# Optimization experiments

Measured on AMD Instinct MI355X. Metric: run time of the kernel, lower is better.

The kernel has to match this reference:

```python
import jax, jax.numpy as jnp
import numpy as np

B, S, D, H, HD, L, E, K, F = 1, 1024, 1024, 16, 64, 64, 8, 2, 4096
EPS = 1e-6


def rms_norm(x):
    return x / jnp.sqrt(jnp.mean(x * x, axis=-1, keepdims=True) + EPS)


def rope_sincos(seq, dim):
    # standard GPT-NeoX-style rotary tables, shape [seq, dim]
    inv = 1.0 / (10000.0 ** (jnp.arange(0, dim, 2, dtype=jnp.float32) / dim))
    ang = jnp.arange(seq, dtype=jnp.float32)[:, None] * inv[None, :]
    sin = jnp.concatenate([jnp.sin(ang), jnp.sin(ang)], axis=-1)
    cos = jnp.concatenate([jnp.cos(ang), jnp.cos(ang)], axis=-1)
    return sin, cos


def apply_rotary(x, sin, cos):
    d = x.shape[-1] // 2
    rot = jnp.concatenate([-x[..., d:], x[..., :d]], axis=-1)
    return x * cos + rot * sin


def setup_inputs() -> dict:
    key = jax.random.key(0)
    ks = jax.random.split(key, 16)
    sd = 0.02

    def nrm(k, shp):
        return jax.random.normal(k, shp, jnp.float32) * sd

    return dict(
        x=jax.random.normal(ks[0], (B, S, D), jnp.float32),
        noise_u=jax.random.uniform(ks[1], (B, S, E), jnp.float32),
        Wdkv=nrm(ks[2], (H, L, HD)),      # per-head w_dkv  (torch weight [L,HD])
        Wq=nrm(ks[3], (H, HD, HD)),       # per-head wq
        Wuv=nrm(ks[4], (H, L, HD)),       # per-head w_uv
        Wuk=nrm(ks[5], (H, L, HD)),       # per-head w_uk
        Wk_rope=nrm(ks[6], (H, L, HD)),   # per-head w_k_rope
        Wq_rope=nrm(ks[7], (H, HD, L)),   # per-head w_q_rope weight
        bq_rope=jnp.zeros((H, HD), jnp.float32),  # w_q_rope bias (Linear default bias=True)
        Wo_head=nrm(ks[8], (H, HD, HD)),  # per-head w_o (no bias)
        Wr=nrm(ks[9], (E, D)),            # router weight
        Wn=nrm(ks[10], (E, D)),           # noise weight
        r_bias=jnp.zeros((E,), jnp.float32),
        W1=nrm(ks[11], (E, D, F)),        # expert fc1 (transposed torch layout)
        b1=jnp.zeros((E, F), jnp.float32),
        W2=nrm(ks[12], (E, F, D)),        # expert fc2
        b2=jnp.zeros((E, D), jnp.float32),
    )


def reference(x, noise_u, Wdkv, Wq, Wuv, Wuk, Wk_rope, Wq_rope, bq_rope,
              Wo_head, Wr, Wn, r_bias, W1, b1, W2, b2):
    # ---- multi-head latent attention (vectorized over heads) ----
    y = rms_norm(x)
    xs = y.reshape(B, S, H, HD).transpose(0, 2, 1, 3)  # [B,H,S,HD]
    sin_k, cos_k = rope_sincos(S, L)
    sin_q, cos_q = rope_sincos(S, HD)

    k = apply_rotary(jnp.einsum('bhsd,hld->bhsl', xs, Wk_rope), sin_k, cos_k)  # [B,H,S,L]
    ckv = jnp.einsum('bhsd,hld->bhsl', xs, Wdkv)                               # [B,H,S,L]
    q = jnp.einsum('bhsl,hdl->bhsd', ckv, Wq_rope) + bq_rope[None, :, None, :]
    q = apply_rotary(q, sin_q, cos_q)                                          # [B,H,S,HD]

    absorbed = jnp.einsum('hqe,hle->hql', Wq, Wuk)                             # [H,HD,L]
    s1 = jnp.einsum('bhsd,hdl,bhtl->bhst', xs, absorbed, ckv)
    s2 = jnp.einsum('bhsd,bhtd->bhst', q, k)
    scores = (s1 + s2) / jnp.sqrt(jnp.float32(2 * HD))
    mask = jnp.tril(jnp.ones((S, S), dtype=bool))  # past_length = 0
    scores = jnp.where(mask, scores, -jnp.inf)
    attn = jax.nn.softmax(scores, axis=-1)

    v = jnp.einsum('bhsl,hld->bhsd', ckv, Wuv)
    o = jnp.einsum('bhst,bhtd->bhsd', attn, v)
    o = jnp.einsum('bhsd,hed->bhse', o, Wo_head)  # per-head w_o (no bias)
    attn_out = o.transpose(0, 2, 1, 3).reshape(B, S, D)
    x = x + attn_out

    # ---- noisy top-k MoE ----
    y2 = rms_norm(x)
    logits = jnp.einsum('bsd,ed->bse', y2, Wr)
    noisy = jnp.einsum('bsd,ed->bse', y2, Wn)
    nl = noise_u * jax.nn.softplus(noisy) + logits + r_bias
    topv, topi = jax.lax.top_k(nl, K)
    gates = jax.nn.softmax(topv, axis=-1)  # softmax over -inf-scattered logits == softmax over top-k
    probs = jnp.sum(gates[..., None] * jax.nn.one_hot(topi, E, dtype=x.dtype), axis=-2)  # [B,S,E]

    h = jax.nn.gelu(jnp.einsum('bsd,edf->ebsf', y2, W1) + b1[:, None, None, :], approximate=False)
    eo = jnp.einsum('ebsf,efd->ebsd', h, W2) + b2[:, None, None, :]
    moe_out = jnp.einsum('bse,ebsd->bsd', probs, eo)
    return x + moe_out
```

## Files before the change

### kernel.cpp

```cpp
#include <hip/hip_runtime.h>
#include <math.h>

#define S_ 1024
#define D_ 1024
#define H_ 16
#define F_ 4096

typedef short s16x8 __attribute__((ext_vector_type(8)));
typedef float fx4 __attribute__((ext_vector_type(4)));

__device__ __forceinline__ float bf2f(unsigned int u){
  union { float f; unsigned int u; } v; v.u = u<<16; return v.f;
}
__device__ __forceinline__ unsigned short f2bf(float f){
  union { float f; unsigned int u; } v; v.f = f;
  unsigned int r = v.u + 0x7fffu + ((v.u>>16)&1u);
  return (unsigned short)(r>>16);
}
__device__ __forceinline__ unsigned int pk2(float a, float b){
  return (unsigned int)f2bf(a) | ((unsigned int)f2bf(b)<<16);
}
__device__ __forceinline__ void gld16(const void* g, void* l){
  typedef const unsigned int __attribute__((address_space(1)))* gp_t;
  typedef unsigned int __attribute__((address_space(3)))* lp_t;
  __builtin_amdgcn_global_load_lds((gp_t)g, (lp_t)l, 16, 0, 0);
}

__global__ __launch_bounds__(256) void k_rmsnorm(const float* __restrict__ x, unsigned short* __restrict__ y){
  int row = blockIdx.x, t = threadIdx.x;
  const float4 v = ((const float4*)(x + (size_t)row*D_))[t];
  float ss = v.x*v.x + v.y*v.y + v.z*v.z + v.w*v.w;
  #pragma unroll
  for(int o=1;o<64;o<<=1) ss += __shfl_xor(ss, o);
  __shared__ float red[4];
  if((t&63)==0) red[t>>6]=ss;
  __syncthreads();
  float sc = rsqrtf((red[0]+red[1]+red[2]+red[3])*(1.0f/D_) + 1e-6f);
  ushort4 o4;
  o4.x=f2bf(v.x*sc); o4.y=f2bf(v.y*sc); o4.z=f2bf(v.z*sc); o4.w=f2bf(v.w*sc);
  ((ushort4*)(y + (size_t)row*D_))[t]=o4;
}

__global__ __launch_bounds__(256) void k_prep(const float* __restrict__ Wq,
    const float* __restrict__ Wuk, const float* __restrict__ Wuv,
    float* __restrict__ abs_t, float* __restrict__ wuvt){
  int h = blockIdx.x, tid = threadIdx.x;
  __shared__ float wq[4096], wuk[4096];
  for(int i=tid;i<4096;i+=256){ wq[i]=Wq[h*4096+i]; wuk[i]=Wuk[h*4096+i]; }
  __syncthreads();
  for(int i=tid;i<4096;i+=256){
    float a=0.f;
    #pragma unroll 8
    for(int e=0;e<64;e++) a += wq[(i&63)*64+e]*wuk[(i>>6)*64+e];
    abs_t[h*4096+i]=a;
    wuvt[h*4096+i]=Wuv[h*4096 + (i&63)*64 + (i>>6)];
  }
}

__device__ __forceinline__ void stage_B64(const float* __restrict__ W, unsigned short* Bs, int tid){
  int n = tid>>2, kq = tid&3;
  const float* s = W + n*64 + kq*16;
  float4 f0=*(const float4*)(s), f1=*(const float4*)(s+4), f2=*(const float4*)(s+8), f3=*(const float4*)(s+12);
  ushort4 u0,u1,u2,u3;
  u0.x=f2bf(f0.x);u0.y=f2bf(f0.y);u0.z=f2bf(f0.z);u0.w=f2bf(f0.w);
  u1.x=f2bf(f1.x);u1.y=f2bf(f1.y);u1.z=f2bf(f1.z);u1.w=f2bf(f1.w);
  u2.x=f2bf(f2.x);u2.y=f2bf(f2.y);u2.z=f2bf(f2.z);u2.w=f2bf(f2.w);
  u3.x=f2bf(f3.x);u3.y=f2bf(f3.y);u3.z=f2bf(f3.z);u3.w=f2bf(f3.w);
  int sl0=((kq*2)^(n&7))*8, sl1=((kq*2+1)^(n&7))*8;
  *(ushort4*)&Bs[n*64+sl0]=u0;   *(ushort4*)&Bs[n*64+sl0+4]=u1;
  *(ushort4*)&Bs[n*64+sl1]=u2;   *(ushort4*)&Bs[n*64+sl1+4]=u3;
}
__device__ __forceinline__ void gemm64(const unsigned short* Asrc, const unsigned short* Bs,
    int wv, int l16, int l4, fx4 acc[4]){
  int srow = wv*16 + l16;
  #pragma unroll
  for(int kb=0;kb<2;kb++){
    s16x8 af = *(const s16x8*)&Asrc[srow*64 + (((kb*4+l4)^(srow&7))*8)];
    #pragma unroll
    for(int nf=0;nf<4;nf++){
      int n = nf*16+l16;
      s16x8 bf = *(const s16x8*)&Bs[n*64 + (((kb*4+l4)^(n&7))*8)];
      acc[nf] = __builtin_amdgcn_mfma_f32_16x16x32_bf16(af, bf, acc[nf], 0,0,0);
    }
  }
}

__global__ __launch_bounds__(256) void k_proj_m(const unsigned short* __restrict__ y,
    const float* __restrict__ abs_t, const float* __restrict__ wuvt,
    const float* __restrict__ Wdkv, const float* __restrict__ Wk_rope,
    const float* __restrict__ Wq_rope, const float* __restrict__ bq_rope,
    unsigned short* __restrict__ kk, unsigned short* __restrict__ qq,
    unsigned short* __restrict__ vv){
  __shared__ unsigned short ysd[4096];
  __shared__ unsigned short ckvs[4096];
  __shared__ unsigned short Bs[4096];
  __shared__ unsigned short tmp[64*72];
  const float LNC = 0.28782313662425575f;
  const float ASC = 0.08838834764831845f;
  int s0 = blockIdx.x*64, h = blockIdx.y, tid = threadIdx.x;
  int wv = tid>>6, lane = tid&63, l16 = lane&15, l4 = lane>>4;
  fx4 acc[4];

  {
    int rg = lane>>3, sg = (lane&7)^(rg&7);
    #pragma unroll
    for(int c2=0;c2<2;c2++){
      int c = wv*2+c2;
      gld16(y + (size_t)(s0+c*8+rg)*D_ + h*64 + sg*8, &ysd[c*512]);
    }
  }
  stage_B64(Wdkv + h*4096, Bs, tid);
  __syncthreads();

  #pragma unroll
  for(int nf=0;nf<4;nf++){acc[nf][0]=0.f;acc[nf][1]=0.f;acc[nf][2]=0.f;acc[nf][3]=0.f;}
  gemm64(ysd, Bs, wv, l16, l4, acc);
  #pragma unroll
  for(int nf=0;nf<4;nf++){
    int col = nf*16+l16;
    #pragma unroll
    for(int r=0;r<4;r++){
      int srow = wv*16+4*l4+r;
      ckvs[srow*64 + (((col>>3)^(srow&7))*8) + (col&7)] = f2bf(acc[nf][r]);
    }
  }
  __syncthreads();
  { int row=tid>>2, sl=(tid&3)*2;
    uint4 a=*(const uint4*)&ckvs[row*64+sl*8];
    uint4 b=*(const uint4*)&ckvs[row*64+sl*8+8];
    unsigned short* kr = kk + ((size_t)(h*S_)+s0+row)*128;
    *(uint4*)&kr[(sl^(row&7))*8]=a;
    *(uint4*)&kr[((sl+1)^(row&7))*8]=b;
  }
  stage_B64(Wk_rope + h*4096, Bs, tid);
  __syncthreads();

  #pragma unroll
  for(int nf=0;nf<4;nf++){acc[nf][0]=0.f;acc[nf][1]=0.f;acc[nf][2]=0.f;acc[nf][3]=0.f;}
  gemm64(ysd, Bs, wv, l16, l4, acc);
  #pragma unroll
  for(int nf=0;nf<2;nf++){
    int llo = nf*16+l16;
    float inv = __expf(-(float)llo * LNC);
    #pragma unroll
    for(int r=0;r<4;r++){
      int srow = wv*16+4*l4+r;
      float sn,cs; __sincosf((float)(s0+srow)*inv,&sn,&cs);
      float alo=acc[nf][r], ahi=acc[nf+2][r];
      tmp[srow*72 + llo]      = f2bf(alo*cs - ahi*sn);
      tmp[srow*72 + llo + 32] = f2bf(ahi*cs + alo*sn);
    }
  }
  __syncthreads();
  { int row=tid>>2, c=(tid&3)*16;
    uint4 a=*(const uint4*)&tmp[row*72+c]; uint4 b=*(const uint4*)&tmp[row*72+c+8];
    unsigned short* kr = kk + ((size_t)(h*S_)+s0+row)*128 + 64;
    *(uint4*)&kr[c]=a; *(uint4*)&kr[c+8]=b; }
  stage_B64(Wq_rope + h*4096, Bs, tid);
  __syncthreads();

  #pragma unroll
  for(int nf=0;nf<4;nf++){acc[nf][0]=0.f;acc[nf][1]=0.f;acc[nf][2]=0.f;acc[nf][3]=0.f;}
  gemm64(ckvs, Bs, wv, l16, l4, acc);
  #pragma unroll
  for(int nf=0;nf<4;nf++){
    float bq = bq_rope[h*64 + nf*16+l16];
    #pragma unroll
    for(int r=0;r<4;r++) acc[nf][r]+=bq;
  }
  #pragma unroll
  for(int nf=0;nf<2;nf++){
    int dlo = nf*16+l16;
    float inv = __expf(-(float)dlo * LNC);
    #pragma unroll
    for(int r=0;r<4;r++){
      int srow = wv*16+4*l4+r;
      float sn,cs; __sincosf((float)(s0+srow)*inv,&sn,&cs);
      float alo=acc[nf][r]*ASC, ahi=acc[nf+2][r]*ASC;
      tmp[srow*72 + dlo]      = f2bf(alo*cs - ahi*sn);
      tmp[srow*72 + dlo + 32] = f2bf(ahi*cs + alo*sn);
    }
  }
  __syncthreads();
  { int row=tid>>2, c=(tid&3)*16;
    uint4 a=*(const uint4*)&tmp[row*72+c]; uint4 b=*(const uint4*)&tmp[row*72+c+8];
    unsigned short* qr = qq + ((size_t)(h*S_)+s0+row)*128 + 64;
    *(uint4*)&qr[c]=a; *(uint4*)&qr[c+8]=b; }
  stage_B64(abs_t + h*4096, Bs, tid);
  __syncthreads();

  #pragma unroll
  for(int nf=0;nf<4;nf++){acc[nf][0]=0.f;acc[nf][1]=0.f;acc[nf][2]=0.f;acc[nf][3]=0.f;}
  gemm64(ysd, Bs, wv, l16, l4, acc);
  #pragma unroll
  for(int nf=0;nf<4;nf++)
    #pragma unroll
    for(int r=0;r<4;r++)
      tmp[(wv*16+4*l4+r)*72 + nf*16+l16] = f2bf(acc[nf][r]*ASC);
  __syncthreads();
  { int row=tid>>2, c=(tid&3)*16;
    uint4 a=*(const uint4*)&tmp[row*72+c]; uint4 b=*(const uint4*)&tmp[row*72+c+8];
    unsigned short* qr = qq + ((size_t)(h*S_)+s0+row)*128;
    *(uint4*)&qr[c]=a; *(uint4*)&qr[c+8]=b; }
  stage_B64(wuvt + h*4096, Bs, tid);
  __syncthreads();

  #pragma unroll
  for(int nf=0;nf<4;nf++){acc[nf][0]=0.f;acc[nf][1]=0.f;acc[nf][2]=0.f;acc[nf][3]=0.f;}
  gemm64(ckvs, Bs, wv, l16, l4, acc);
  #pragma unroll
  for(int nf=0;nf<4;nf++)
    #pragma unroll
    for(int r=0;r<4;r++)
      tmp[(wv*16+4*l4+r)*72 + nf*16+l16] = f2bf(acc[nf][r]);
  __syncthreads();
  { int row=tid>>2, c=(tid&3)*16;
    uint4 a=*(const uint4*)&tmp[row*72+c]; uint4 b=*(const uint4*)&tmp[row*72+c+8];
    unsigned short* vr = vv + ((size_t)(h*S_)+s0+row)*64;
    *(uint4*)&vr[c]=a; *(uint4*)&vr[c+8]=b; }
}

__global__ __launch_bounds__(256) void k_attn2(const unsigned short* __restrict__ qq,
    const unsigned short* __restrict__ kk, const unsigned short* __restrict__ vv,
    const float* __restrict__ Wo, const float* __restrict__ x, float* __restrict__ x1){
  __shared__ unsigned short Ks[64*128];
  __shared__ unsigned short Vt[64*72];
  __shared__ unsigned short Pl[4][16*72];
  int h = blockIdx.y, q0 = blockIdx.x*64, tid = threadIdx.x;
  int wave = tid>>6, lane = tid&63;
  int l16 = lane&15, l4 = lane>>4;
  int qglob = q0 + wave*16 + l16;

  s16x8 qf[4];
  {
    const unsigned short* qp = qq + ((size_t)(h*S_)+qglob)*128 + l4*8;
    #pragma unroll
    for(int kb=0;kb<4;kb++) qf[kb] = *(const s16x8*)(qp + kb*32);
  }
  fx4 ot[4];
  #pragma unroll
  for(int t=0;t<4;t++){ ot[t][0]=0.f; ot[t][1]=0.f; ot[t][2]=0.f; ot[t][3]=0.f; }
  float mrun=-1e30f, lrun=0.f;
  int nkt = blockIdx.x + 1;

  for(int kt=0;kt<nkt;kt++){
    int kt0 = kt*64;
    __syncthreads();
    #pragma unroll
    for(int it=0;it<4;it++){
      int idx = tid + it*256;
      int row = idx>>4, c = idx&15;
      uint4 u = *(const uint4*)(kk + ((size_t)(h*S_)+kt0+row)*128 + c*8);
      *(uint4*)&Ks[row*128 + ((c^(row&7))<<3)] = u;
    }
    #pragma unroll
    for(int it=0;it<2;it++){
      int idx = tid + it*256;
      int k = idx>>3, d0 = (idx&7)*8;
      uint4 u = *(const uint4*)(vv + ((size_t)(h*S_)+kt0+k)*64 + d0);
      unsigned short t8[8];
      *(uint4*)t8 = u;
      #pragma unroll
      for(int j=0;j<8;j++) Vt[(d0+j)*72 + k] = t8[j];
    }
    __syncthreads();

    fx4 sa[4];
    #pragma unroll
    for(int i=0;i<4;i++){ sa[i][0]=0.f; sa[i][1]=0.f; sa[i][2]=0.f; sa[i][3]=0.f; }
    #pragma unroll
    for(int kb=0;kb<4;kb++){
      #pragma unroll
      for(int i=0;i<4;i++){
        int row = 16*i + l16;
        s16x8 ak = *(const s16x8*)&Ks[row*128 + (((l4+4*kb)^(row&7))<<3)];
        sa[i] = __builtin_amdgcn_mfma_f32_16x16x32_bf16(ak, qf[kb], sa[i], 0,0,0);
      }
    }
    float pv[16]; float mloc=-1e30f;
    #pragma unroll
    for(int i=0;i<4;i++)
      #pragma unroll
      for(int r=0;r<4;r++){
        int kg = kt0 + 16*i + 4*l4 + r;
        float s = (kg<=qglob)? sa[i][r] : -1e30f;
        pv[i*4+r]=s; mloc=fmaxf(mloc,s);
      }
    mloc = fmaxf(mloc, __shfl_xor(mloc,16));
    mloc = fmaxf(mloc, __shfl_xor(mloc,32));
    float mnew = fmaxf(mrun,mloc);
    float alpha = __expf(mrun-mnew);
    float psum=0.f;
    #pragma unroll
    for(int z=0;z<16;z++){ pv[z]=__expf(pv[z]-mnew); psum+=pv[z]; }
    psum += __shfl_xor(psum,16); psum += __shfl_xor(psum,32);
    lrun = lrun*alpha + psum; mrun = mnew;
    #pragma unroll
    for(int t=0;t<4;t++){ ot[t][0]*=alpha; ot[t][1]*=alpha; ot[t][2]*=alpha; ot[t][3]*=alpha; }
    {
      unsigned short* pw = &Pl[wave][l16*72 + 4*l4];
      #pragma unroll
      for(int i=0;i<4;i++){
        *(unsigned int*)&pw[16*i]   = pk2(pv[i*4+0],pv[i*4+1]);
        *(unsigned int*)&pw[16*i+2] = pk2(pv[i*4+2],pv[i*4+3]);
      }
    }
    #pragma unroll
    for(int kb=0;kb<2;kb++){
      s16x8 pf = *(const s16x8*)&Pl[wave][l16*72 + kb*32 + l4*8];
      #pragma unroll
      for(int t=0;t<4;t++){
        s16x8 av = *(const s16x8*)&Vt[(16*t+l16)*72 + kb*32 + l4*8];
        ot[t] = __builtin_amdgcn_mfma_f32_16x16x32_bf16(av, pf, ot[t], 0,0,0);
      }
    }
  }

  float invl = 1.f/lrun;
  {
    unsigned short* pw = &Pl[wave][l16*72 + 4*l4];
    #pragma unroll
    for(int t=0;t<4;t++){
      *(unsigned int*)&pw[16*t]   = pk2(ot[t][0]*invl, ot[t][1]*invl);
      *(unsigned int*)&pw[16*t+2] = pk2(ot[t][2]*invl, ot[t][3]*invl);
    }
  }
  __syncthreads();
  #pragma unroll
  for(int it=0;it<4;it++){
    int idx = tid + it*256;
    int ee = idx>>4, dd = (idx&15)*4;
    float4 wv = *(const float4*)(Wo + h*4096 + ee*64 + dd);
    ushort4 w4; w4.x=f2bf(wv.x); w4.y=f2bf(wv.y); w4.z=f2bf(wv.z); w4.w=f2bf(wv.w);
    *(ushort4*)&Vt[ee*72 + dd] = w4;
  }
  __syncthreads();
  fx4 outT[4];
  #pragma unroll
  for(int t=0;t<4;t++){ outT[t][0]=0.f; outT[t][1]=0.f; outT[t][2]=0.f; outT[t][3]=0.f; }
  #pragma unroll
  for(int kb=0;kb<2;kb++){
    s16x8 of = *(const s16x8*)&Pl[wave][l16*72 + kb*32 + l4*8];
    #pragma unroll
    for(int t=0;t<4;t++){
      s16x8 aw = *(const s16x8*)&Vt[(16*t+l16)*72 + kb*32 + l4*8];
      outT[t] = __builtin_amdgcn_mfma_f32_16x16x32_bf16(aw, of, outT[t], 0,0,0);
    }
  }
  #pragma unroll
  for(int t=0;t<4;t++){
    size_t base = (size_t)qglob*D_ + h*64 + 16*t + 4*l4;
    float4 xv = *(const float4*)(x + base);
    float4 r;
    r.x = xv.x + outT[t][0]; r.y = xv.y + outT[t][1];
    r.z = xv.z + outT[t][2]; r.w = xv.w + outT[t][3];
    *(float4*)(x1+base) = r;
  }
}

__global__ __launch_bounds__(64) void k_gate(const float* __restrict__ x1, const float* __restrict__ Wr,
    const float* __restrict__ Wn, const float* __restrict__ r_bias, const float* __restrict__ noise_u,
    float* __restrict__ gates, int* __restrict__ topi){
  int s = blockIdx.x, lane = threadIdx.x;
  const float* xr = x1 + (size_t)s*D_ + lane*16;
  float yv[16]; float ss=0.f;
  #pragma unroll
  for(int i=0;i<16;i+=4){
    float4 a = *(const float4*)(xr+i);
    yv[i]=a.x; yv[i+1]=a.y; yv[i+2]=a.z; yv[i+3]=a.w;
    ss += a.x*a.x+a.y*a.y+a.z*a.z+a.w*a.w;
  }
  #pragma unroll
  for(int o=1;o<64;o<<=1) ss += __shfl_xor(ss,o);
  float sc = rsqrtf(ss*(1.0f/D_) + 1e-6f);
  #pragma unroll
  for(int i=0;i<16;i++) yv[i]*=sc;
  float lg[8], nz[8];
  #pragma unroll
  for(int e=0;e<8;e++){
    const float* wr = Wr + e*D_ + lane*16;
    const float* wn = Wn + e*D_ + lane*16;
    float a=0.f,b=0.f;
    #pragma unroll
    for(int i=0;i<16;i+=4){
      float4 w1 = *(const float4*)(wr+i); float4 w2 = *(const float4*)(wn+i);
      a += yv[i]*w1.x + yv[i+1]*w1.y + yv[i+2]*w1.z + yv[i+3]*w1.w;
      b += yv[i]*w2.x + yv[i+1]*w2.y + yv[i+2]*w2.z + yv[i+3]*w2.w;
    }
    lg[e]=a; nz[e]=b;
  }
  #pragma unroll
  for(int o=1;o<64;o<<=1){
    #pragma unroll
    for(int e=0;e<8;e++){ lg[e]+=__shfl_xor(lg[e],o); nz[e]+=__shfl_xor(nz[e],o); }
  }
  if(lane==0){
    float nl[8];
    for(int e=0;e<8;e++){
      float z = nz[e];
      float sp = (z>20.f)? z : log1pf(expf(z));
      nl[e] = noise_u[s*8+e]*sp + lg[e] + r_bias[e];
    }
    int i0=0; float v0=nl[0];
    for(int e=1;e<8;e++) if(nl[e]>v0){v0=nl[e];i0=e;}
    float v1=-1e30f; int i1=0;
    for(int e=0;e<8;e++) if(e!=i0 && nl[e]>v1){v1=nl[e];i1=e;}
    float ex = expf(v1-v0);
    gates[s*2]   = 1.f/(1.f+ex);
    gates[s*2+1] = ex/(1.f+ex);
    topi[s*2]=i0; topi[s*2+1]=i1;
  }
}

__global__ __launch_bounds__(256) void k_lists(const int* __restrict__ topi,
    int* __restrict__ offs, int* __restrict__ pair_tok, int* __restrict__ slot_of){
  __shared__ int tp[2048];
  __shared__ int cnt[8];
  __shared__ int off_s[9];
  int t = threadIdx.x;
  int wave = t>>6, lane = t&63;
  unsigned long long below = (lane==63)? 0xFFFFFFFFFFFFFFFFull>>1
                                       : ((1ull<<lane)-1ull);
  for(int i=t;i<2048;i+=256) tp[i]=topi[i];
  __syncthreads();
  #pragma unroll
  for(int sub=0;sub<2;sub++){
    int e = wave*2+sub;
    int c=0;
    for(int ch=0;ch<32;ch++) c += (tp[ch*64+lane]==e);
    #pragma unroll
    for(int o=1;o<64;o<<=1) c += __shfl_xor(c,o);
    if(lane==0) cnt[e]=c;
  }
  __syncthreads();
  if(t==0){
    int a=0;
    for(int e=0;e<8;e++){ off_s[e]=a; a += (cnt[e]+127)&~127; }
    off_s[8]=a;
    for(int e=0;e<9;e++) offs[e]=off_s[e];
  }
  __syncthreads();
  #pragma unroll
  for(int sub=0;sub<2;sub++){
    int e = wave*2+sub;
    int base = off_s[e];
    for(int ch=0;ch<32;ch++){
      int idx = ch*64+lane;
      bool pred = (tp[idx]==e);
      unsigned long long mask = __ballot(pred);
      if(pred){
        int slot = base + __popcll(mask & below);
        pair_tok[slot] = idx>>1;
        slot_of[idx] = slot;
      }
      base += __popcll(mask);
    }
    for(int slot=base+lane; slot<off_s[e+1]; slot+=64) pair_tok[slot]=0;
  }
}

__global__ __launch_bounds__(256) void k_cvt_t(const float* __restrict__ src,
    unsigned short* __restrict__ dst, int R, int C){
  __shared__ float ts[64][65];
  int e = blockIdx.z;
  int r0 = blockIdx.x*64, c0 = blockIdx.y*64;
  const float* s = src + (size_t)e*R*C;
  unsigned short* d = dst + (size_t)e*R*C;
  int t = threadIdx.x;
  #pragma unroll
  for(int it=0; it<4; it++){
    int flat = it*256+t;
    int r = flat>>4, cq = (flat&15)*4;
    float4 v = *(const float4*)(s + (size_t)(r0+r)*C + c0+cq);
    ts[r][cq]=v.x; ts[r][cq+1]=v.y; ts[r][cq+2]=v.z; ts[r][cq+3]=v.w;
  }
  __syncthreads();
  #pragma unroll
  for(int it=0; it<4; it++){
    int flat = it*256+t;
    int c = flat>>4, kq = (flat&15)*4;
    ushort4 o;
    o.x=f2bf(ts[kq][c]); o.y=f2bf(ts[kq+1][c]); o.z=f2bf(ts[kq+2][c]); o.w=f2bf(ts[kq+3][c]);
    *(ushort4*)(d + (size_t)(c0+c)*R + r0+kq) = o;
  }
}

__global__ __launch_bounds__(256) void k_fc1t(const unsigned short* __restrict__ y2,
    const int* __restrict__ pair_tok, const int* __restrict__ offs,
    const unsigned short* __restrict__ Bt, const float* __restrict__ bias1,
    unsigned short* __restrict__ hbuf){
  __shared__ unsigned short As[2][8192];
  __shared__ unsigned short Bs[2][8192];
  __shared__ int sh_e;
  int tid=threadIdx.x, lane=tid&63, wv=tid>>6;
  int r0=blockIdx.x*128, n0=blockIdx.y*128;
  if(tid==0){ int e=-1; if(r0<offs[8]){e=0; while(offs[e+1]<=r0) e++;} sh_e=e; }
  __syncthreads();
  int e=sh_e; if(e<0) return;
  int rg = lane>>3;
  int sg = (lane&7)^(rg&7);
  const unsigned short* aptr[4];
  const unsigned short* bptr[4];
  #pragma unroll
  for(int c=0;c<4;c++){
    int ch = wv*4+c;
    int tok = pair_tok[r0 + ch*8 + rg];
    aptr[c] = y2 + (size_t)tok*D_ + sg*8;
    bptr[c] = Bt + (size_t)e*D_*F_ + (size_t)(n0 + ch*8 + rg)*D_ + sg*8;
  }
  int l16=lane&15, l4=lane>>4;
  int wm=wv>>1, wn=wv&1;
  fx4 acc[4][4];
  #pragma unroll
  for(int a0=0;a0<4;a0++)
    #pragma unroll
    for(int b0=0;b0<4;b0++){ acc[a0][b0][0]=0.f; acc[a0][b0][1]=0.f; acc[a0][b0][2]=0.f; acc[a0][b0][3]=0.f; }

  #pragma unroll
  for(int c=0;c<4;c++){
    gld16(aptr[c], &As[0][(wv*4+c)*512]);
    gld16(bptr[c], &Bs[0][(wv*4+c)*512]);
  }

  int buf=0;
  for(int kt=0;kt<D_-64;kt+=64){
    #pragma unroll
    for(int c=0;c<4;c++){
      gld16(aptr[c]+kt+64, &As[buf^1][(wv*4+c)*512]);
      gld16(bptr[c]+kt+64, &Bs[buf^1][(wv*4+c)*512]);
    }
    asm volatile("s_waitcnt vmcnt(8)" ::: "memory");
    asm volatile("s_barrier" ::: "memory");
    #pragma unroll
    for(int kb=0;kb<2;kb++){
      s16x8 af[4], bf8[4];
      #pragma unroll
      for(int mf=0;mf<4;mf++){
        int row = wm*64+mf*16+l16;
        af[mf] = *(const s16x8*)&As[buf][row*64 + (((kb*4+l4)^(row&7))*8)];
      }
      #pragma unroll
      for(int nf=0;nf<4;nf++){
        int col = wn*64+nf*16+l16;
        bf8[nf] = *(const s16x8*)&Bs[buf][col*64 + (((kb*4+l4)^(col&7))*8)];
      }
      #pragma unroll
      for(int mf=0;mf<4;mf++)
        #pragma unroll
        for(int nf=0;nf<4;nf++)
          acc[mf][nf]=__builtin_amdgcn_mfma_f32_16x16x32_bf16(af[mf],bf8[nf],acc[mf][nf],0,0,0);
    }
    asm volatile("s_barrier" ::: "memory");
    buf ^= 1;
  }
  asm volatile("s_waitcnt vmcnt(0)" ::: "memory");
  asm volatile("s_barrier" ::: "memory");
  #pragma unroll
  for(int kb=0;kb<2;kb++){
    s16x8 af[4], bf8[4];
    #pragma unroll
    for(int mf=0;mf<4;mf++){
      int row = wm*64+mf*16+l16;
      af[mf] = *(const s16x8*)&As[buf][row*64 + (((kb*4+l4)^(row&7))*8)];
    }
    #pragma unroll
    for(int nf=0;nf<4;nf++){
      int col = wn*64+nf*16+l16;
      bf8[nf] = *(const s16x8*)&Bs[buf][col*64 + (((kb*4+l4)^(col&7))*8)];
    }
    #pragma unroll
    for(int mf=0;mf<4;mf++)
      #pragma unroll
      for(int nf=0;nf<4;nf++)
        acc[mf][nf]=__builtin_amdgcn_mfma_f32_16x16x32_bf16(af[mf],bf8[nf],acc[mf][nf],0,0,0);
  }
  #pragma unroll
  for(int mf=0;mf<4;mf++)
    #pragma unroll
    for(int nf=0;nf<4;nf++){
      int gcol=n0+wn*64+nf*16+l16;
      float bias=bias1[e*F_+gcol];
      #pragma unroll
      for(int rgi=0;rgi<4;rgi++){
        int grow=r0+wm*64+mf*16+l4*4+rgi;
        float vv=acc[mf][nf][rgi]+bias;
        float g=0.5f*vv*(1.f+erff(vv*0.70710678118654752f));
        hbuf[(size_t)grow*F_+gcol]=f2bf(g);
      }
    }
}

__global__ __launch_bounds__(256) void k_fc2t(const unsigned short* __restrict__ hbuf,
    const int* __restrict__ offs, const unsigned short* __restrict__ Bt,
    const float* __restrict__ bias2, float* __restrict__ eo, int klen){
  __shared__ unsigned short As[2][8192];
  __shared__ unsigned short Bs[2][4096];
  __shared__ int sh_e;
  int tid=threadIdx.x, lane=tid&63, wv=tid>>6;
  int r0=blockIdx.x*128, n0=blockIdx.y*64;
  int k0=blockIdx.z*klen;
  if(tid==0){ int e=-1; if(r0<offs[8]){e=0; while(offs[e+1]<=r0) e++;} sh_e=e; }
  __syncthreads();
  int e=sh_e; if(e<0) return;
  int rg = lane>>3;
  int sg = (lane&7)^(rg&7);
  const unsigned short* aptr[4];
  const unsigned short* bptr[2];
  #pragma unroll
  for(int c=0;c<4;c++){
    int ch = wv*4+c;
    aptr[c] = hbuf + (size_t)(r0 + ch*8 + rg)*F_ + k0 + sg*8;
  }
  #pragma unroll
  for(int c=0;c<2;c++){
    int ch = wv*2+c;
    bptr[c] = Bt + (size_t)e*F_*D_ + (size_t)(n0 + ch*8 + rg)*F_ + k0 + sg*8;
  }
  int l16=lane&15, l4=lane>>4;
  fx4 acc[2][4];
  #pragma unroll
  for(int a0=0;a0<2;a0++)
    #pragma unroll
    for(int b0=0;b0<4;b0++){ acc[a0][b0][0]=0.f; acc[a0][b0][1]=0.f; acc[a0][b0][2]=0.f; acc[a0][b0][3]=0.f; }

  #pragma unroll
  for(int c=0;c<4;c++) gld16(aptr[c], &As[0][(wv*4+c)*512]);
  #pragma unroll
  for(int c=0;c<2;c++) gld16(bptr[c], &Bs[0][(wv*2+c)*512]);

  int buf=0;
  for(int kt=0;kt<klen-64;kt+=64){
    #pragma unroll
    for(int c=0;c<4;c++) gld16(aptr[c]+kt+64, &As[buf^1][(wv*4+c)*512]);
    #pragma unroll
    for(int c=0;c<2;c++) gld16(bptr[c]+kt+64, &Bs[buf^1][(wv*2+c)*512]);
    asm volatile("s_waitcnt vmcnt(6)" ::: "memory");
    asm volatile("s_barrier" ::: "memory");
    #pragma unroll
    for(int kb=0;kb<2;kb++){
      s16x8 af[2], bf8[4];
      #pragma unroll
      for(int mf=0;mf<2;mf++){
        int row = wv*32+mf*16+l16;
        af[mf] = *(const s16x8*)&As[buf][row*64 + (((kb*4+l4)^(row&7))*8)];
      }
      #pragma unroll
      for(int nf=0;nf<4;nf++){
        int col = nf*16+l16;
        bf8[nf] = *(const s16x8*)&Bs[buf][col*64 + (((kb*4+l4)^(col&7))*8)];
      }
      #pragma unroll
      for(int mf=0;mf<2;mf++)
        #pragma unroll
        for(int nf=0;nf<4;nf++)
          acc[mf][nf]=__builtin_amdgcn_mfma_f32_16x16x32_bf16(af[mf],bf8[nf],acc[mf][nf],0,0,0);
    }
    asm volatile("s_barrier" ::: "memory");
    buf ^= 1;
  }
  asm volatile("s_waitcnt vmcnt(0)" ::: "memory");
  asm volatile("s_barrier" ::: "memory");
  #pragma unroll
  for(int kb=0;kb<2;kb++){
    s16x8 af[2], bf8[4];
    #pragma unroll
    for(int mf=0;mf<2;mf++){
      int row = wv*32+mf*16+l16;
      af[mf] = *(const s16x8*)&As[buf][row*64 + (((kb*4+l4)^(row&7))*8)];
    }
    #pragma unroll
    for(int nf=0;nf<4;nf++){
      int col = nf*16+l16;
      bf8[nf] = *(const s16x8*)&Bs[buf][col*64 + (((kb*4+l4)^(col&7))*8)];
    }
    #pragma unroll
    for(int mf=0;mf<2;mf++)
      #pragma unroll
      for(int nf=0;nf<4;nf++)
        acc[mf][nf]=__builtin_amdgcn_mfma_f32_16x16x32_bf16(af[mf],bf8[nf],acc[mf][nf],0,0,0);
  }
  float* eop = eo + (size_t)blockIdx.z*3072*D_;
  #pragma unroll
  for(int mf=0;mf<2;mf++)
    #pragma unroll
    for(int nf=0;nf<4;nf++){
      int gcol=n0+nf*16+l16;
      float bias=(blockIdx.z==0)? bias2[e*D_+gcol] : 0.f;
      #pragma unroll
      for(int rgi=0;rgi<4;rgi++){
        int grow=r0+wv*32+mf*16+l4*4+rgi;
        eop[(size_t)grow*D_+gcol]=acc[mf][nf][rgi]+bias;
      }
    }
}

__global__ __launch_bounds__(256) void k_fc1_fb(const unsigned short* __restrict__ y2,
    const int* __restrict__ pair_tok, const int* __restrict__ offs,
    const float* __restrict__ W1, const float* __restrict__ bias1,
    unsigned short* __restrict__ hbuf){
  __shared__ unsigned short As[4096];
  __shared__ unsigned short Bs[4096];
  __shared__ int sh_e;
  int tid=threadIdx.x;
  int r0=blockIdx.x*128, n0=blockIdx.y*128;
  if(tid==0){ int e=-1; if(r0<offs[8]){ e=0; while(offs[e+1]<=r0) e++; } sh_e=e; }
  __syncthreads();
  int e=sh_e; if(e<0) return;
  const float* Bsrc = W1 + (size_t)e*D_*F_;
  int r=tid&127, hf=tid>>7;
  int tok=pair_tok[r0+r];
  const unsigned short* Asrc = y2 + (size_t)tok*D_ + hf*16;
  int pk=tid>>5, pn=tid&31;
  int lane=tid&63, wvid=tid>>6;
  int wm=wvid>>1, wn=wvid&1;
  int l16=lane&15, l4=lane>>4;
  fx4 acc[4][4];
  #pragma unroll
  for(int a0=0;a0<4;a0++)
    #pragma unroll
    for(int b0=0;b0<4;b0++){ acc[a0][b0][0]=0.f; acc[a0][b0][1]=0.f; acc[a0][b0][2]=0.f; acc[a0][b0][3]=0.f; }
  for(int kt=0;kt<D_;kt+=32){
    uint4 av0=*(const uint4*)(Asrc+kt);
    uint4 av1=*(const uint4*)(Asrc+kt+8);
    const float* bp=Bsrc+(size_t)(kt+pk*4)*F_+n0+pn*4;
    float4 bv0=*(const float4*)(bp);
    float4 bv1=*(const float4*)(bp+F_);
    float4 bv2=*(const float4*)(bp+2*F_);
    float4 bv3=*(const float4*)(bp+3*F_);
    *(uint4*)&As[(hf*2)*1024 + r*8]=av0;
    *(uint4*)&As[(hf*2+1)*1024 + r*8]=av1;
    unsigned short c0[4]={f2bf(bv0.x),f2bf(bv0.y),f2bf(bv0.z),f2bf(bv0.w)};
    unsigned short c1[4]={f2bf(bv1.x),f2bf(bv1.y),f2bf(bv1.z),f2bf(bv1.w)};
    unsigned short c2[4]={f2bf(bv2.x),f2bf(bv2.y),f2bf(bv2.z),f2bf(bv2.w)};
    unsigned short c3[4]={f2bf(bv3.x),f2bf(bv3.y),f2bf(bv3.z),f2bf(bv3.w)};
    #pragma unroll
    for(int j2=0;j2<4;j2++){
      int col=pn*4+j2;
      int kb=(pk*4)^(((col>>2)&3)<<3);
      ushort4 wr;
      wr.x=c0[j2]; wr.y=c1[j2]; wr.z=c2[j2]; wr.w=c3[j2];
      *(ushort4*)&Bs[col*32+kb]=wr;
    }
    __syncthreads();
    s16x8 af[4],bf8[4];
    #pragma unroll
    for(int mf=0;mf<4;mf++){
      int rowl=wm*64+mf*16+l16;
      af[mf]=*(const s16x8*)&As[l4*1024+rowl*8];
    }
    #pragma unroll
    for(int nf=0;nf<4;nf++){
      int col=wn*64+nf*16+l16;
      int kb=(l4*8)^(((col>>2)&3)<<3);
      bf8[nf]=*(const s16x8*)&Bs[col*32+kb];
    }
    #pragma unroll
    for(int mf=0;mf<4;mf++)
      #pragma unroll
      for(int nf=0;nf<4;nf++)
        acc[mf][nf]=__builtin_amdgcn_mfma_f32_16x16x32_bf16(af[mf],bf8[nf],acc[mf][nf],0,0,0);
    __syncthreads();
  }
  #pragma unroll
  for(int mf=0;mf<4;mf++)
    #pragma unroll
    for(int nf=0;nf<4;nf++){
      int gcol=n0+wn*64+nf*16+l16;
      float bias=bias1[e*F_+gcol];
      #pragma unroll
      for(int rg=0;rg<4;rg++){
        int grow=r0+wm*64+mf*16+l4*4+rg;
        float vv=acc[mf][nf][rg]+bias;
        float g=0.5f*vv*(1.f+erff(vv*0.70710678118654752f));
        hbuf[(size_t)grow*F_+gcol]=f2bf(g);
      }
    }
}

__global__ __launch_bounds__(256) void k_fc2_fb(const unsigned short* __restrict__ hbuf,
    const int* __restrict__ offs, const float* __restrict__ W2,
    const float* __restrict__ bias2, float* __restrict__ eo){
  __shared__ unsigned short As[4096];
  __shared__ unsigned short Bs[2048];
  __shared__ int sh_e;
  int tid=threadIdx.x;
  int r0=blockIdx.x*128, n0=blockIdx.y*64;
  if(tid==0){ int e=-1; if(r0<offs[8]){ e=0; while(offs[e+1]<=r0) e++; } sh_e=e; }
  __syncthreads();
  int e=sh_e; if(e<0) return;
  const float* Bsrc=W2+(size_t)e*F_*D_;
  int r=tid&127, hf=tid>>7;
  const unsigned short* Asrc=hbuf+(size_t)(r0+r)*F_+hf*16;
  int pk=tid>>4, pn=tid&15;
  int lane=tid&63, wvid=tid>>6;
  int l16=lane&15, l4=lane>>4;
  fx4 acc[2][4];
  #pragma unroll
  for(int a0=0;a0<2;a0++)
    #pragma unroll
    for(int b0=0;b0<4;b0++){ acc[a0][b0][0]=0.f; acc[a0][b0][1]=0.f; acc[a0][b0][2]=0.f; acc[a0][b0][3]=0.f; }
  for(int kt=0;kt<F_;kt+=32){
    uint4 av0=*(const uint4*)(Asrc+kt);
    uint4 av1=*(const uint4*)(Asrc+kt+8);
    const float* bp=Bsrc+(size_t)(kt+pk*2)*D_+n0+pn*4;
    float4 bv0=*(const float4*)bp;
    float4 bv1=*(const float4*)(bp+D_);
    *(uint4*)&As[(hf*2)*1024+r*8]=av0;
    *(uint4*)&As[(hf*2+1)*1024+r*8]=av1;
    unsigned short c0[4]={f2bf(bv0.x),f2bf(bv0.y),f2bf(bv0.z),f2bf(bv0.w)};
    unsigned short c1[4]={f2bf(bv1.x),f2bf(bv1.y),f2bf(bv1.z),f2bf(bv1.w)};
    #pragma unroll
    for(int j2=0;j2<4;j2++){
      int col=pn*4+j2;
      int kb=(pk*2)^(((col>>2)&3)<<3);
      unsigned int pack=(unsigned int)c0[j2] | ((unsigned int)c1[j2]<<16);
      *(unsigned int*)&Bs[col*32+kb]=pack;
    }
    __syncthreads();
    s16x8 af[2],bf8[4];
    #pragma unroll
    for(int mf=0;mf<2;mf++){
      int rowl=wvid*32+mf*16+l16;
      af[mf]=*(const s16x8*)&As[l4*1024+rowl*8];
    }
    #pragma unroll
    for(int nf=0;nf<4;nf++){
      int col=nf*16+l16;
      int kb=(l4*8)^(((col>>2)&3)<<3);
      bf8[nf]=*(const s16x8*)&Bs[col*32+kb];
    }
    #pragma unroll
    for(int mf=0;mf<2;mf++)
      #pragma unroll
      for(int nf=0;nf<4;nf++)
        acc[mf][nf]=__builtin_amdgcn_mfma_f32_16x16x32_bf16(af[mf],bf8[nf],acc[mf][nf],0,0,0);
    __syncthreads();
  }
  #pragma unroll
  for(int mf=0;mf<2;mf++)
    #pragma unroll
    for(int nf=0;nf<4;nf++){
      int gcol=n0+nf*16+l16;
      float bias=bias2[e*D_+gcol];
      #pragma unroll
      for(int rg=0;rg<4;rg++){
        int grow=r0+wvid*32+mf*16+l4*4+rg;
        eo[(size_t)grow*D_+gcol]=acc[mf][nf][rg]+bias;
      }
    }
}

__global__ __launch_bounds__(256) void k_combine(const float* __restrict__ x1, const float* __restrict__ eo,
    int parts, const float* __restrict__ gates, const int* __restrict__ slot_of, float* __restrict__ out){
  int s=blockIdx.x, t=threadIdx.x;
  float g0=gates[s*2], g1=gates[s*2+1];
  int a0=slot_of[s*2], a1=slot_of[s*2+1];
  float4 o=((const float4*)(x1+(size_t)s*D_))[t];
  for(int p=0;p<parts;p++){
    const float* ep = eo + (size_t)p*3072*D_;
    float4 e0=((const float4*)(ep+(size_t)a0*D_))[t];
    float4 e1=((const float4*)(ep+(size_t)a1*D_))[t];
    o.x+=g0*e0.x+g1*e1.x;
    o.y+=g0*e0.y+g1*e1.y;
    o.z+=g0*e0.z+g1*e1.z;
    o.w+=g0*e0.w+g1*e1.w;
  }
  ((float4*)(out+(size_t)s*D_))[t]=o;
}

extern "C" void kernel_launch(void* const* d_in, const int* in_sizes, int n_in,
                              void* d_out, int out_size, void* d_ws, size_t ws_size,
                              hipStream_t stream){
  (void)in_sizes; (void)n_in; (void)out_size;
  const float* x       = (const float*)d_in[0];
  const float* noise_u = (const float*)d_in[1];
  const float* Wdkv    = (const float*)d_in[2];
  const float* Wq      = (const float*)d_in[3];
  const float* Wuv     = (const float*)d_in[4];
  const float* Wuk     = (const float*)d_in[5];
  const float* Wk_rope = (const float*)d_in[6];
  const float* Wq_rope = (const float*)d_in[7];
  const float* bq_rope = (const float*)d_in[8];
  const float* Wo_head = (const float*)d_in[9];
  const float* Wr      = (const float*)d_in[10];
  const float* Wn      = (const float*)d_in[11];
  const float* r_bias  = (const float*)d_in[12];
  const float* W1      = (const float*)d_in[13];
  const float* b1      = (const float*)d_in[14];
  const float* W2      = (const float*)d_in[15];
  const float* b2      = (const float*)d_in[16];
  float* out           = (float*)d_out;

  char* w = (char*)d_ws;
  unsigned short* y    = (unsigned short*)(w);
  unsigned short* kk   = (unsigned short*)(w + 2097152);
  unsigned short* qq   = (unsigned short*)(w + 6291456);
  unsigned short* vv   = (unsigned short*)(w + 10485760);
  float* abs_t         = (float*)(w + 12582912);
  float* wuvt          = (float*)(w + 12845056);
  float* x1            = (float*)(w + 13107200);
  unsigned short* y2   = (unsigned short*)(w + 17301504);
  float* gates         = (float*)(w + 19398656);
  int* topi            = (int*)(w + 19406848);
  int* slot_of         = (int*)(w + 19415040);
  int* offs            = (int*)(w + 19423232);
  int* pair_tok        = (int*)(w + 19427328);
  unsigned short* hbuf = (unsigned short*)(w + 19443712);
  float* eo            = (float*)(w + 44609536);

  const size_t NEED4 = 162050048ull;
  const size_t NEED2 = 136884224ull;
  int parts; unsigned short* Wt;
  if(ws_size >= NEED4){ parts = 4; Wt = (unsigned short*)(w + 94941184); }
  else if(ws_size >= NEED2){ parts = 2; Wt = (unsigned short*)(w + 69775360); }
  else { parts = 0; Wt = 0; }

  if(parts){
    k_cvt_t<<<dim3(16,64,8),256,0,stream>>>(W1, Wt, D_, F_);
  }
  k_rmsnorm<<<S_,256,0,stream>>>(x, y);
  k_prep<<<H_,256,0,stream>>>(Wq, Wuk, Wuv, abs_t, wuvt);
  k_proj_m<<<dim3(16,H_),256,0,stream>>>(y, abs_t, wuvt, Wdkv, Wk_rope, Wq_rope, bq_rope, kk, qq, vv);
  k_attn2<<<dim3(16,H_),256,0,stream>>>(qq, kk, vv, Wo_head, x, x1);
  k_rmsnorm<<<S_,256,0,stream>>>(x1, y2);
  k_gate<<<S_,64,0,stream>>>(x1, Wr, Wn, r_bias, noise_u, gates, topi);
  k_lists<<<1,256,0,stream>>>(topi, offs, pair_tok, slot_of);
  if(parts){
    k_fc1t<<<dim3(24,32),256,0,stream>>>(y2, pair_tok, offs, Wt, b1, hbuf);
    k_cvt_t<<<dim3(64,16,8),256,0,stream>>>(W2, Wt, F_, D_);
    k_fc2t<<<dim3(24,16,parts),256,0,stream>>>(hbuf, offs, Wt, b2, eo, F_/parts);
    k_combine<<<S_,256,0,stream>>>(x1, eo, parts, gates, slot_of, out);
  } else {
    k_fc1_fb<<<dim3(24,32),256,0,stream>>>(y2, pair_tok, offs, W1, b1, hbuf);
    k_fc2_fb<<<dim3(24,16),256,0,stream>>>(hbuf, offs, W2, b2, eo);
    k_combine<<<S_,256,0,stream>>>(x1, eo, 1, gates, slot_of, out);
  }
}
```

Before: 318.7 us.

## Fuse second RMSNorm into gate kernel, XCD-swizzle MoE GEMM grids, raise MFMA priority

The gate kernel now writes the normalized bf16 activations itself, so the separate rmsnorm launch over x1 is removed. The fc1 and fc2 expert GEMMs switch to 1D grids with an XCD-aware block remap, so neighbouring tiles land on the same chiplet and share L2. MFMA sections are wrapped in s_setprio to favour compute waves over load issue. The remap assumes the block count divides evenly by 8, and the fallback path is unchanged.

```diff
diff --git a/kernel.cpp b/kernel.cpp
--- a/kernel.cpp
+++ b/kernel.cpp
@@ -24,6 +24,10 @@
   typedef const unsigned int __attribute__((address_space(1)))* gp_t;
   typedef unsigned int __attribute__((address_space(3)))* lp_t;
   __builtin_amdgcn_global_load_lds((gp_t)g, (lp_t)l, 16, 0, 0);
+}
+__device__ __forceinline__ int xcd_swz(int bid, int nwg){
+  int q = nwg >> 3;
+  return (bid & 7)*q + (bid >> 3);
 }
 
 __global__ __launch_bounds__(256) void k_rmsnorm(const float* __restrict__ x, unsigned short* __restrict__ y){
@@ -360,7 +364,7 @@
 
 __global__ __launch_bounds__(64) void k_gate(const float* __restrict__ x1, const float* __restrict__ Wr,
     const float* __restrict__ Wn, const float* __restrict__ r_bias, const float* __restrict__ noise_u,
-    float* __restrict__ gates, int* __restrict__ topi){
+    float* __restrict__ gates, int* __restrict__ topi, unsigned short* __restrict__ y2){
   int s = blockIdx.x, lane = threadIdx.x;
   const float* xr = x1 + (size_t)s*D_ + lane*16;
   float yv[16]; float ss=0.f;
@@ -375,6 +379,16 @@
   float sc = rsqrtf(ss*(1.0f/D_) + 1e-6f);
   #pragma unroll
   for(int i=0;i<16;i++) yv[i]*=sc;
+  {
+    unsigned short* yo = y2 + (size_t)s*D_ + lane*16;
+    ushort4 o0,o1,o2,o3;
+    o0.x=f2bf(yv[0]); o0.y=f2bf(yv[1]); o0.z=f2bf(yv[2]); o0.w=f2bf(yv[3]);
+    o1.x=f2bf(yv[4]); o1.y=f2bf(yv[5]); o1.z=f2bf(yv[6]); o1.w=f2bf(yv[7]);
+    o2.x=f2bf(yv[8]); o2.y=f2bf(yv[9]); o2.z=f2bf(yv[10]); o2.w=f2bf(yv[11]);
+    o3.x=f2bf(yv[12]); o3.y=f2bf(yv[13]); o3.z=f2bf(yv[14]); o3.w=f2bf(yv[15]);
+    *(ushort4*)(yo)   = o0; *(ushort4*)(yo+4) = o1;
+    *(ushort4*)(yo+8) = o2; *(ushort4*)(yo+12)= o3;
+  }
   float lg[8], nz[8];
   #pragma unroll
   for(int e=0;e<8;e++){
@@ -493,7 +507,8 @@
   __shared__ unsigned short Bs[2][8192];
   __shared__ int sh_e;
   int tid=threadIdx.x, lane=tid&63, wv=tid>>6;
-  int r0=blockIdx.x*128, n0=blockIdx.y*128;
+  int swz = xcd_swz(blockIdx.x, 768);
+  int r0 = (swz % 24)*128, n0 = (swz / 24)*128;
   if(tid==0){ int e=-1; if(r0<offs[8]){e=0; while(offs[e+1]<=r0) e++;} sh_e=e; }
   __syncthreads();
   int e=sh_e; if(e<0) return;
@@ -531,6 +546,7 @@
     }
     asm volatile("s_waitcnt vmcnt(8)" ::: "memory");
     asm volatile("s_barrier" ::: "memory");
+    __builtin_amdgcn_s_setprio(1);
     #pragma unroll
     for(int kb=0;kb<2;kb++){
       s16x8 af[4], bf8[4];
@@ -550,11 +566,13 @@
         for(int nf=0;nf<4;nf++)
           acc[mf][nf]=__builtin_amdgcn_mfma_f32_16x16x32_bf16(af[mf],bf8[nf],acc[mf][nf],0,0,0);
     }
+    __builtin_amdgcn_s_setprio(0);
     asm volatile("s_barrier" ::: "memory");
     buf ^= 1;
   }
   asm volatile("s_waitcnt vmcnt(0)" ::: "memory");
   asm volatile("s_barrier" ::: "memory");
+  __builtin_amdgcn_s_setprio(1);
   #pragma unroll
   for(int kb=0;kb<2;kb++){
     s16x8 af[4], bf8[4];
@@ -574,6 +592,7 @@
       for(int nf=0;nf<4;nf++)
         acc[mf][nf]=__builtin_amdgcn_mfma_f32_16x16x32_bf16(af[mf],bf8[nf],acc[mf][nf],0,0,0);
   }
+  __builtin_amdgcn_s_setprio(0);
   #pragma unroll
   for(int mf=0;mf<4;mf++)
     #pragma unroll
@@ -592,13 +611,17 @@
 
 __global__ __launch_bounds__(256) void k_fc2t(const unsigned short* __restrict__ hbuf,
     const int* __restrict__ offs, const unsigned short* __restrict__ Bt,
-    const float* __restrict__ bias2, float* __restrict__ eo, int klen){
+    const float* __restrict__ bias2, float* __restrict__ eo, int klen, int parts){
   __shared__ unsigned short As[2][8192];
   __shared__ unsigned short Bs[2][4096];
   __shared__ int sh_e;
   int tid=threadIdx.x, lane=tid&63, wv=tid>>6;
-  int r0=blockIdx.x*128, n0=blockIdx.y*64;
-  int k0=blockIdx.z*klen;
+  int nwg = 384*parts;
+  int swz = xcd_swz(blockIdx.x, nwg);
+  int kz  = swz / 384;
+  int rem = swz % 384;
+  int r0 = (rem % 24)*128, n0 = (rem / 24)*64;
+  int k0 = kz*klen;
   if(tid==0){ int e=-1; if(r0<offs[8]){e=0; while(offs[e+1]<=r0) e++;} sh_e=e; }
   __syncthreads();
   int e=sh_e; if(e<0) return;
@@ -636,6 +659,7 @@
     for(int c=0;c<2;c++) gld16(bptr[c]+kt+64, &Bs[buf^1][(wv*2+c)*512]);
     asm volatile("s_waitcnt vmcnt(6)" ::: "memory");
     asm volatile("s_barrier" ::: "memory");
+    __builtin_amdgcn_s_setprio(1);
     #pragma unroll
     for(int kb=0;kb<2;kb++){
       s16x8 af[2], bf8[4];
@@ -655,11 +679,13 @@
         for(int nf=0;nf<4;nf++)
           acc[mf][nf]=__builtin_amdgcn_mfma_f32_16x16x32_bf16(af[mf],bf8[nf],acc[mf][nf],0,0,0);
     }
+    __builtin_amdgcn_s_setprio(0);
     asm volatile("s_barrier" ::: "memory");
     buf ^= 1;
   }
   asm volatile("s_waitcnt vmcnt(0)" ::: "memory");
   asm volatile("s_barrier" ::: "memory");
+  __builtin_amdgcn_s_setprio(1);
   #pragma unroll
   for(int kb=0;kb<2;kb++){
     s16x8 af[2], bf8[4];
@@ -679,13 +705,14 @@
       for(int nf=0;nf<4;nf++)
         acc[mf][nf]=__builtin_amdgcn_mfma_f32_16x16x32_bf16(af[mf],bf8[nf],acc[mf][nf],0,0,0);
   }
-  float* eop = eo + (size_t)blockIdx.z*3072*D_;
+  __builtin_amdgcn_s_setprio(0);
+  float* eop = eo + (size_t)kz*3072*D_;
   #pragma unroll
   for(int mf=0;mf<2;mf++)
     #pragma unroll
     for(int nf=0;nf<4;nf++){
       int gcol=n0+nf*16+l16;
-      float bias=(blockIdx.z==0)? bias2[e*D_+gcol] : 0.f;
+      float bias=(kz==0)? bias2[e*D_+gcol] : 0.f;
       #pragma unroll
       for(int rgi=0;rgi<4;rgi++){
         int grow=r0+wv*32+mf*16+l4*4+rgi;
@@ -922,13 +949,12 @@
   k_prep<<<H_,256,0,stream>>>(Wq, Wuk, Wuv, abs_t, wuvt);
   k_proj_m<<<dim3(16,H_),256,0,stream>>>(y, abs_t, wuvt, Wdkv, Wk_rope, Wq_rope, bq_rope, kk, qq, vv);
   k_attn2<<<dim3(16,H_),256,0,stream>>>(qq, kk, vv, Wo_head, x, x1);
-  k_rmsnorm<<<S_,256,0,stream>>>(x1, y2);
-  k_gate<<<S_,64,0,stream>>>(x1, Wr, Wn, r_bias, noise_u, gates, topi);
+  k_gate<<<S_,64,0,stream>>>(x1, Wr, Wn, r_bias, noise_u, gates, topi, y2);
   k_lists<<<1,256,0,stream>>>(topi, offs, pair_tok, slot_of);
   if(parts){
-    k_fc1t<<<dim3(24,32),256,0,stream>>>(y2, pair_tok, offs, Wt, b1, hbuf);
+    k_fc1t<<<768,256,0,stream>>>(y2, pair_tok, offs, Wt, b1, hbuf);
     k_cvt_t<<<dim3(64,16,8),256,0,stream>>>(W2, Wt, F_, D_);
-    k_fc2t<<<dim3(24,16,parts),256,0,stream>>>(hbuf, offs, Wt, b2, eo, F_/parts);
+    k_fc2t<<<384*parts,256,0,stream>>>(hbuf, offs, Wt, b2, eo, F_/parts, parts);
     k_combine<<<S_,256,0,stream>>>(x1, eo, parts, gates, slot_of, out);
   } else {
     k_fc1_fb<<<dim3(24,32),256,0,stream>>>(y2, pair_tok, offs, W1, b1, hbuf);
```

Measured after the change: 303.5 us. -4.7%, faster.
